# Kernel optimization log

Measured on AMD Instinct MI355X. Metric: run time of the kernel, lower is better.

Reference implementation:

```python
import jax, jax.numpy as jnp
import numpy as np

B, S, D = 16, 38, 1792          # batch, seq_len, d_model = 768 + 2*512
H, DK = 4, 448                   # heads, head dim (D // H)
NP = 128                         # prototype rows before repeat
TOPK = 3                         # hard-coded in VqaPrototypeModel
INF = 768                        # qamodel.qa_outputs.in_features


def setup_inputs() -> dict:
    key = jax.random.key(0)
    ks = jax.random.split(key, 16)
    sc = lambda d: 1.0 / np.sqrt(d)
    inp = {
        "combined_features": jax.random.normal(ks[0], (B, S, D), jnp.float32),
        "prototype_vectors": jax.random.normal(ks[1], (1, NP, D), jnp.float32),
        "attention_mask": jnp.ones((B, S), jnp.int32),
        # MultiThreadMemory: 4 Linear(d_model, d_model) -> q, k, v, out
        "Wq": jax.random.normal(ks[2], (D, D), jnp.float32) * sc(D),
        "bq": jnp.zeros((D,), jnp.float32),
        "Wk": jax.random.normal(ks[3], (D, D), jnp.float32) * sc(D),
        "bk": jnp.zeros((D,), jnp.float32),
        "Wv": jax.random.normal(ks[4], (D, D), jnp.float32) * sc(D),
        "bv": jnp.zeros((D,), jnp.float32),
        "Wo": jax.random.normal(ks[5], (D, D), jnp.float32) * sc(D),
        "bo": jnp.zeros((D,), jnp.float32),
        # fc: Linear(2*d_model, in_features)
        "Wfc": jax.random.normal(ks[6], (2 * D, INF), jnp.float32) * sc(2 * D),
        "bfc": jnp.zeros((INF,), jnp.float32),
        # stub of qamodel.qa_outputs: Linear(in_features, 2)
        "Wqa": jax.random.normal(ks[7], (INF, 2), jnp.float32) * sc(INF),
        "bqa": jnp.zeros((2,), jnp.float32),
    }
    return inp


def reference(combined_features, prototype_vectors, attention_mask,
              Wq, bq, Wk, bk, Wv, bv, Wo, bo, Wfc, bfc, Wqa, bqa):
    b, s, d = combined_features.shape
    # prototype_vectors.repeat(batch_size, seq_length, 1) -> [B, S*NP, D]
    pv = jnp.tile(prototype_vectors, (b, s, 1))
    m = pv.shape[1]

    q = combined_features @ Wq + bq                     # [B,S,D]
    k = pv @ Wk + bk                                    # [B,M,D]
    v = pv @ Wv + bv                                    # [B,M,D]

    q = q.reshape(b, s, H, DK).transpose(0, 2, 1, 3)    # [B,H,S,DK]
    k = k.reshape(b, m, H, DK).transpose(0, 2, 1, 3)    # [B,H,M,DK]
    v = v.reshape(b, m, H, DK).transpose(0, 2, 1, 3)    # [B,H,M,DK]

    # memory_querying_responding: score + topk + gather + softmax + weighted sum
    scores = jnp.einsum('bhsd,bhmd->bhsm', q, k) / np.sqrt(DK)  # [B,H,S,M]
    sel_scores, idx = jax.lax.top_k(scores, TOPK)               # [B,H,S,TOPK]
    # gather selected prototype values: v[b,h,idx[b,h,s,:],:]
    sel_value = jnp.take_along_axis(v[:, :, None, :, :], idx[..., None], axis=3)
    # sel_value: [B,H,S,TOPK,DK]
    p_attn = jax.nn.softmax(sel_scores.astype(jnp.float32), axis=-1)
    x = jnp.einsum('bhsk,bhskd->bhsd', p_attn, sel_value)       # [B,H,S,DK]
    x = x.transpose(0, 2, 1, 3).reshape(b, s, H * DK)           # [B,S,D]
    response = x @ Wo + bo

    final = jnp.concatenate([combined_features, response], axis=2)  # [B,S,2D]
    reduced = final @ Wfc + bfc                                     # [B,S,INF]
    # qamodel stub: qa_outputs head -> start/end logits stacked on last dim
    logits = reduced @ Wqa + bqa                                    # [B,S,2]
    return logits
```

## Files before the change

### kernel.cpp

```cpp
#include <hip/hip_runtime.h>

typedef __attribute__((ext_vector_type(8))) short short8v;
typedef __attribute__((ext_vector_type(4))) float f32x4;

#define APL 5120
#define BPL 5184
#define BBASE 15360

struct SP {
    const float *p0, *p1, *p2, *p3, *p4, *p5, *p6, *p7;
    float *q0, *q1, *q2;
};

__device__ __forceinline__ float wave_sum(float v) {
    #pragma unroll
    for (int off = 32; off; off >>= 1) v += __shfl_down(v, off);
    return v;
}

__device__ __forceinline__ void colvec2_unit(
    const float* __restrict__ A, int lda, const float* __restrict__ W,
    float* __restrict__ out, int K, int m, int lane)
{
    const float4* a = (const float4*)(A + (long)m * lda);
    float a0 = 0.f, a1 = 0.f;
    for (int i = 0; i < K / 256; ++i) {
        const int d4 = lane + 64 * i;
        float4 xv = a[d4];
        const float4* w = (const float4*)(W + (long)d4 * 8);
        float4 w0 = w[0], w1 = w[1];
        a0 += xv.x*w0.x + xv.y*w0.z + xv.z*w1.x + xv.w*w1.z;
        a1 += xv.x*w0.y + xv.y*w0.w + xv.z*w1.y + xv.w*w1.w;
    }
    a0 = wave_sum(a0); a1 = wave_sum(a1);
    if (lane == 0) { out[m * 2 + 0] = a0; out[m * 2 + 1] = a1; }
}

__device__ __forceinline__ void sbias_unit(
    const float* __restrict__ bq, const float* __restrict__ Kp,
    float* __restrict__ sb, int unit, int lane)
{
    const int h = unit >> 7, p = unit & 127;
    const float* kr = Kp + (long)p * 1792 + h * 448;
    const float* bh = bq + h * 448;
    float s = 0.f;
    #pragma unroll
    for (int i = 0; i < 7; ++i) s = fmaf(bh[lane + 64 * i], kr[lane + 64 * i], s);
    s = wave_sum(s);
    if (lane == 0) sb[unit] = s;
}

__device__ __forceinline__ void wvwoq_unit(
    const float* __restrict__ Wv, const float* __restrict__ WoQ,
    float* __restrict__ out, int d, int h, int lane)
{
    const float* wr = Wv + (long)d * 1792 + h * 448;
    const float* wq = WoQ + h * 448 * 2;
    float s0 = 0.f, s1 = 0.f;
    #pragma unroll
    for (int i = 0; i < 7; ++i) {
        const int j = lane + 64 * i;
        const float v = wr[j];
        s0 = fmaf(v, wq[j * 2 + 0], s0);
        s1 = fmaf(v, wq[j * 2 + 1], s1);
    }
    s0 = wave_sum(s0); s1 = wave_sum(s1);
    if (lane == 0) {
        out[((long)h * 1792 + d) * 2 + 0] = s0;
        out[((long)h * 1792 + d) * 2 + 1] = s1;
    }
}

__device__ __forceinline__ void bias_unit(
    const float* __restrict__ bv, const float* __restrict__ WoQ,
    const float* __restrict__ bfc, const float* __restrict__ Wqa,
    const float* __restrict__ bo, const float* __restrict__ WfbQ,
    const float* __restrict__ bqa,
    float* __restrict__ cv, float* __restrict__ const2, int unit, int lane)
{
    float s0 = 0.f, s1 = 0.f;
    if (unit < 4) {
        const int h = unit;
        #pragma unroll
        for (int i = 0; i < 7; ++i) {
            const int j = h * 448 + lane + 64 * i;
            const float v = bv[j];
            s0 = fmaf(v, WoQ[j * 2 + 0], s0);
            s1 = fmaf(v, WoQ[j * 2 + 1], s1);
        }
    } else {
        for (int k = lane; k < 1792; k += 64) {
            if (k < 768) {
                s0 = fmaf(bfc[k], Wqa[k * 2 + 0], s0);
                s1 = fmaf(bfc[k], Wqa[k * 2 + 1], s1);
            }
            s0 = fmaf(bo[k], WfbQ[k * 2 + 0], s0);
            s1 = fmaf(bo[k], WfbQ[k * 2 + 1], s1);
        }
    }
    s0 = wave_sum(s0); s1 = wave_sum(s1);
    if (lane == 0) {
        if (unit < 4) { cv[unit * 2 + 0] = s0; cv[unit * 2 + 1] = s1; }
        else          { const2[0] = s0 + bqa[0]; const2[1] = s1 + bqa[1]; }
    }
}

__device__ __forceinline__ void split3(float f, unsigned& h, unsigned& m, unsigned& l) {
    unsigned u = __float_as_uint(f);
    h = u >> 16;
    float r1 = f - __uint_as_float(u & 0xFFFF0000u);
    unsigned u1 = __float_as_uint(r1);
    m = u1 >> 16;
    float r2 = r1 - __uint_as_float(u1 & 0xFFFF0000u);
    l = __float_as_uint(r2) >> 16;
}

__device__ __forceinline__ int BROWF(int n) { return n * 40 + (n >> 4) * 8; }

template<bool TRANSB, int SIDE>
__global__ __launch_bounds__(256) void mgemm(
    const float* __restrict__ A, int lda,
    const float* __restrict__ B, int ldb,
    float* __restrict__ C,
    int M, int N, int K,
    int nsplit, int nbb, int mainZ,
    long sAb, long sBb, SP sp)
{
    const int tid = threadIdx.x;
    if ((int)blockIdx.z >= mainZ) {
        const int bid = ((int)blockIdx.z - mainZ) * (gridDim.x * gridDim.y)
                      + blockIdx.y * gridDim.x + blockIdx.x;
        const int lane = tid & 63;
        const int u = bid * 4 + (tid >> 6);
        if constexpr (SIDE == 1) {
            if (u < 3584) colvec2_unit(sp.p0, 768, sp.p1, sp.q0, 768, u, lane);
        } else if constexpr (SIDE == 2) {
            if (u < 1792)       colvec2_unit(sp.p0, 1792, sp.p1, sp.q0, 1792, u, lane);
            else if (u < 2304)  sbias_unit(sp.p2, sp.p3, sp.q1, u - 1792, lane);
        } else if constexpr (SIDE == 3) {
            if (u < 7168)       wvwoq_unit(sp.p0, sp.p1, sp.q0, u % 1792, u / 1792, lane);
            else if (u < 7173)  bias_unit(sp.p2, sp.p1, sp.p3, sp.p4, sp.p5, sp.p6, sp.p7,
                                          sp.q1, sp.q2, u - 7168, lane);
        }
        return;
    }

    __shared__ unsigned short sh[30912];

    const int kb = blockIdx.z % nsplit;
    const int bb = blockIdx.z / nsplit;
    A += sAb * bb;
    B += sBb * bb;
    const int Kc = K / nsplit;
    const int kbeg = kb * Kc;
    const int nsteps = Kc / 32;

    const int lane = tid & 63, wave = tid >> 6;
    const int g = lane >> 4, c = lane & 15;
    const int wm = (wave >> 1) * 64, wn = (wave & 1) * 64;
    const int rowBase = blockIdx.y * 128;
    const int colBase = blockIdx.x * 128;

    const int s_arow = tid >> 1, s_ak = (tid & 1) * 16;
    const int s_bk = tid >> 3,  s_bn = (tid & 7) * 16;
    const int s_tn = tid >> 1,  s_tk = (tid & 1) * 16;

    const bool aok = (rowBase + s_arow) < M;
    const float* Arow = A + (long)(rowBase + s_arow) * lda;

    float4 ra[4], rb[4];
    auto loadRaw = [&](int ks) {
        const int k0 = kbeg + ks * 32;
        #pragma unroll
        for (int i = 0; i < 4; ++i)
            ra[i] = aok ? *(const float4*)&Arow[k0 + s_ak + i * 4]
                        : make_float4(0.f, 0.f, 0.f, 0.f);
        if (!TRANSB) {
            const float* bp = B + (long)(k0 + s_bk) * ldb + colBase + s_bn;
            #pragma unroll
            for (int i = 0; i < 4; ++i) rb[i] = *(const float4*)&bp[i * 4];
        } else {
            const float* bp = B + (long)(colBase + s_tn) * ldb + k0 + s_tk;
            #pragma unroll
            for (int i = 0; i < 4; ++i) rb[i] = *(const float4*)&bp[i * 4];
        }
    };

    auto stageWrite = [&]() {
        {
            const float* f = (const float*)ra;
            unsigned ph[8], pm[8], pl[8];
            #pragma unroll
            for (int j = 0; j < 8; ++j) {
                unsigned h0, m0, l0, h1, m1, l1;
                split3(f[2*j], h0, m0, l0);
                split3(f[2*j+1], h1, m1, l1);
                ph[j] = h0 | (h1 << 16);
                pm[j] = m0 | (m1 << 16);
                pl[j] = l0 | (l1 << 16);
            }
            const int base = s_arow * 40 + s_ak;
            unsigned short* ap = sh;
            *(uint4*)&ap[0*APL + base]     = make_uint4(ph[0],ph[1],ph[2],ph[3]);
            *(uint4*)&ap[0*APL + base + 8] = make_uint4(ph[4],ph[5],ph[6],ph[7]);
            *(uint4*)&ap[1*APL + base]     = make_uint4(pm[0],pm[1],pm[2],pm[3]);
            *(uint4*)&ap[1*APL + base + 8] = make_uint4(pm[4],pm[5],pm[6],pm[7]);
            *(uint4*)&ap[2*APL + base]     = make_uint4(pl[0],pl[1],pl[2],pl[3]);
            *(uint4*)&ap[2*APL + base + 8] = make_uint4(pl[4],pl[5],pl[6],pl[7]);
        }
        unsigned short* bp = sh + BBASE;
        if (!TRANSB) {
            const float* f = (const float*)rb;
            #pragma unroll
            for (int j = 0; j < 16; ++j) {
                unsigned h, m, l;
                split3(f[j], h, m, l);
                const int ad = BROWF(s_bn + j) + s_bk;
                bp[0*BPL + ad] = (unsigned short)h;
                bp[1*BPL + ad] = (unsigned short)m;
                bp[2*BPL + ad] = (unsigned short)l;
            }
        } else {
            const float* f = (const float*)rb;
            unsigned ph[8], pm[8], pl[8];
            #pragma unroll
            for (int j = 0; j < 8; ++j) {
                unsigned h0, m0, l0, h1, m1, l1;
                split3(f[2*j], h0, m0, l0);
                split3(f[2*j+1], h1, m1, l1);
                ph[j] = h0 | (h1 << 16);
                pm[j] = m0 | (m1 << 16);
                pl[j] = l0 | (l1 << 16);
            }
            const int base = BROWF(s_tn) + s_tk;
            *(uint4*)&bp[0*BPL + base]     = make_uint4(ph[0],ph[1],ph[2],ph[3]);
            *(uint4*)&bp[0*BPL + base + 8] = make_uint4(ph[4],ph[5],ph[6],ph[7]);
            *(uint4*)&bp[1*BPL + base]     = make_uint4(pm[0],pm[1],pm[2],pm[3]);
            *(uint4*)&bp[1*BPL + base + 8] = make_uint4(pm[4],pm[5],pm[6],pm[7]);
            *(uint4*)&bp[2*BPL + base]     = make_uint4(pl[0],pl[1],pl[2],pl[3]);
            *(uint4*)&bp[2*BPL + base + 8] = make_uint4(pl[4],pl[5],pl[6],pl[7]);
        }
    };

    f32x4 acc[4][4];
    #pragma unroll
    for (int i = 0; i < 4; ++i)
        #pragma unroll
        for (int j = 0; j < 4; ++j)
            acc[i][j] = (f32x4){0.f, 0.f, 0.f, 0.f};

    loadRaw(0);
    for (int s = 0; s < nsteps; ++s) {
        __syncthreads();
        stageWrite();
        if (s + 1 < nsteps) loadRaw(s + 1);
        __syncthreads();

        const unsigned short* ap = sh;
        const unsigned short* bp = sh + BBASE;
        short8v bfr[3][4];
        #pragma unroll
        for (int ni = 0; ni < 4; ++ni) {
            const int hwb = (wn + 16*ni + c) * 40 + ((wn + 16*ni) >> 4) * 8 + 8 * g;
            bfr[0][ni] = *(const short8v*)&bp[0*BPL + hwb];
            bfr[1][ni] = *(const short8v*)&bp[1*BPL + hwb];
            bfr[2][ni] = *(const short8v*)&bp[2*BPL + hwb];
        }
        #pragma unroll
        for (int mi = 0; mi < 4; ++mi) {
            const int hwa = (wm + 16*mi + c) * 40 + 8 * g;
            short8v ah = *(const short8v*)&ap[0*APL + hwa];
            short8v am = *(const short8v*)&ap[1*APL + hwa];
            short8v al = *(const short8v*)&ap[2*APL + hwa];
            #pragma unroll
            for (int ni = 0; ni < 4; ++ni) {
                f32x4 t = acc[mi][ni];
                t = __builtin_amdgcn_mfma_f32_16x16x32_bf16(ah, bfr[0][ni], t, 0, 0, 0);
                t = __builtin_amdgcn_mfma_f32_16x16x32_bf16(ah, bfr[1][ni], t, 0, 0, 0);
                t = __builtin_amdgcn_mfma_f32_16x16x32_bf16(am, bfr[0][ni], t, 0, 0, 0);
                t = __builtin_amdgcn_mfma_f32_16x16x32_bf16(ah, bfr[2][ni], t, 0, 0, 0);
                t = __builtin_amdgcn_mfma_f32_16x16x32_bf16(am, bfr[1][ni], t, 0, 0, 0);
                t = __builtin_amdgcn_mfma_f32_16x16x32_bf16(al, bfr[0][ni], t, 0, 0, 0);
                acc[mi][ni] = t;
            }
        }
    }

    float* Cw = C + ((long)kb * nbb + bb) * (long)M * N;
    #pragma unroll
    for (int mi = 0; mi < 4; ++mi)
        #pragma unroll
        for (int ni = 0; ni < 4; ++ni) {
            const int col = colBase + wn + 16*ni + c;
            #pragma unroll
            for (int r = 0; r < 4; ++r) {
                const int row = rowBase + wm + 16*mi + 4*g + r;
                if (row < M) Cw[(long)row * N + col] = acc[mi][ni][r];
            }
        }
}

__global__ __launch_bounds__(256) void reduce_add(
    const float* __restrict__ part, float* __restrict__ out,
    const float* __restrict__ bias, int N, long sz, int nsplit)
{
    long i = (long)blockIdx.x * 256 + threadIdx.x;
    const long stride = (long)gridDim.x * 256;
    for (; i < sz; i += stride) {
        float s = 0.f;
        for (int z = 0; z < nsplit; ++z) s += part[z * sz + i];
        if (bias) s += bias[i % N];
        out[i] = s;
    }
}

__global__ __launch_bounds__(256) void argmax_final_k(
    const float* __restrict__ Sp,
    const float* __restrict__ sbias,
    const float* __restrict__ X, const float* __restrict__ Wbig,
    const float* __restrict__ WvWoQ,
    const float* __restrict__ proto,
    const float* __restrict__ cv, const float* __restrict__ const2,
    float* __restrict__ out)
{
    const int lane = threadIdx.x & 63;
    const int row = blockIdx.x * 4 + (threadIdx.x >> 6);
    if (row >= 608) return;

    int sel[4];
    #pragma unroll
    for (int h = 0; h < 4; ++h) {
        float s0 = sbias[h * 128 + lane];
        float s1 = sbias[h * 128 + lane + 64];
        #pragma unroll
        for (int z = 0; z < 8; ++z) {
            const long base = ((long)(z * 4 + h) * 608 + row) * 128;
            s0 += Sp[base + lane];
            s1 += Sp[base + lane + 64];
        }
        float best = s0; int bi = lane;
        if (s1 > best) { best = s1; bi = lane + 64; }
        #pragma unroll
        for (int off = 32; off; off >>= 1) {
            float ov = __shfl_down(best, off);
            int   oi = __shfl_down(bi, off);
            if (ov > best || (ov == best && oi < bi)) { best = ov; bi = oi; }
        }
        sel[h] = __shfl(bi, 0);
    }

    float a0 = 0.f, a1 = 0.f;
    auto dot2 = [&](const float* a, const float* w) {
        const float4* av = (const float4*)a;
        #pragma unroll
        for (int i = 0; i < 7; ++i) {
            const int d4 = lane + 64 * i;
            float4 xv = av[d4];
            const float4* wp = (const float4*)(w + (long)d4 * 8);
            float4 w0 = wp[0], w1 = wp[1];
            a0 += xv.x*w0.x + xv.y*w0.z + xv.z*w1.x + xv.w*w1.z;
            a1 += xv.x*w0.y + xv.y*w0.w + xv.z*w1.y + xv.w*w1.w;
        }
    };
    dot2(X + (long)row * 1792, Wbig);
    #pragma unroll
    for (int h = 0; h < 4; ++h)
        dot2(proto + (long)sel[h] * 1792, WvWoQ + (long)h * 3584);

    a0 = wave_sum(a0); a1 = wave_sum(a1);
    if (lane == 0) {
        out[row * 2 + 0] = a0 + const2[0] + cv[0] + cv[2] + cv[4] + cv[6];
        out[row * 2 + 1] = a1 + const2[1] + cv[1] + cv[3] + cv[5] + cv[7];
    }
}

extern "C" void kernel_launch(void* const* d_in, const int* in_sizes, int n_in,
                              void* d_out, int out_size, void* d_ws, size_t ws_size,
                              hipStream_t stream)
{
    const float* X     = (const float*)d_in[0];
    const float* proto = (const float*)d_in[1];
    const float* Wq  = (const float*)d_in[3];
    const float* bq  = (const float*)d_in[4];
    const float* Wk  = (const float*)d_in[5];
    const float* bk  = (const float*)d_in[6];
    const float* Wv  = (const float*)d_in[7];
    const float* bv  = (const float*)d_in[8];
    const float* Wo  = (const float*)d_in[9];
    const float* bo  = (const float*)d_in[10];
    const float* Wfc = (const float*)d_in[11];
    const float* bfc = (const float*)d_in[12];
    const float* Wqa = (const float*)d_in[13];
    const float* bqa = (const float*)d_in[14];
    float* out = (float*)d_out;

    float* ws = (float*)d_ws;
    float* P      = ws;
    float* Kp     = P + 3211264;
    float* W2b    = Kp + 229376;
    float* sbias  = W2b + 917504;
    float* WbigB  = sbias + 512;
    float* WoQ    = WbigB + 7168;
    float* WvWoQ  = WoQ + 3584;
    float* cv     = WvWoQ + 14336;
    float* const2 = cv + 8;
    float* WfbQ   = WbigB + 3584;

    dim3 blk(256);

    {
        SP sp{}; sp.p0 = Wfc; sp.p1 = Wqa; sp.q0 = WbigB;
        mgemm<false, 1><<<dim3(14, 1, 14 + 64), blk, 0, stream>>>(
            proto, 1792, Wk, 1792, P, 128, 1792, 1792, 14, 1, 14, 0, 0, sp);
    }
    reduce_add<<<dim3(896), blk, 0, stream>>>(P, Kp, bk, 1792, 229376L, 14);

    {
        SP sp{}; sp.p0 = Wo; sp.p1 = WfbQ; sp.q0 = WoQ; sp.p2 = bq; sp.p3 = Kp; sp.q1 = sbias;
        mgemm<true, 2><<<dim3(1, 14, 8 + 42), blk, 0, stream>>>(
            Wq, 1792, Kp, 1792, P, 1792, 128, 448, 2, 4, 8, 448, 448, sp);
    }
    reduce_add<<<dim3(1792), blk, 0, stream>>>(P, W2b, nullptr, 1, 917504L, 2);

    {
        SP sp{}; sp.p0 = Wv; sp.p1 = WoQ; sp.q0 = WvWoQ;
        sp.p2 = bv; sp.p3 = bfc; sp.p4 = Wqa; sp.p5 = bo; sp.p6 = WfbQ; sp.p7 = bqa;
        sp.q1 = cv; sp.q2 = const2;
        mgemm<false, 3><<<dim3(1, 5, 32 + 359), blk, 0, stream>>>(
            X, 1792, W2b, 128, P, 608, 128, 1792, 8, 4, 32, 0, 229376L, sp);
    }
    argmax_final_k<<<dim3(152), blk, 0, stream>>>(
        P, sbias, X, WbigB, WvWoQ, proto, cv, const2, out);
}
```

Baseline: 81.05 us.

## Fuse all stages into one cooperative persistent kernel with grid syncs

Replaces the six separate kernel launches (three GEMMs with side work plus two reductions and the final argmax) with a single cooperative persistent kernel that runs six phases separated by grid-wide barriers. Work is redistributed: the split-K is raised (14 splits in the last GEMM), and reductions plus side vector products are interleaved inside phases via grid-stride loops. The aim is to remove launch overhead and inter-kernel gaps. It risks grid.sync costs, a grid capped at 448 blocks limiting parallelism, and extra partial-sum traffic. A fallback launches the phases as separate kernels.

```diff
diff --git a/kernel.cpp b/kernel.cpp
--- a/kernel.cpp
+++ b/kernel.cpp
@@ -1,4 +1,7 @@
 #include <hip/hip_runtime.h>
+#include <hip/hip_cooperative_groups.h>
+
+namespace cg = cooperative_groups;
 
 typedef __attribute__((ext_vector_type(8))) short short8v;
 typedef __attribute__((ext_vector_type(4))) float f32x4;
@@ -6,10 +9,11 @@
 #define APL 5120
 #define BPL 5184
 #define BBASE 15360
-
-struct SP {
-    const float *p0, *p1, *p2, *p3, *p4, *p5, *p6, *p7;
-    float *q0, *q1, *q2;
+#define MAXGRID 448
+
+struct MA {
+    const float *X, *proto, *Wq, *bq, *Wk, *bk, *Wv, *bv, *Wo, *bo, *Wfc, *bfc, *Wqa, *bqa;
+    float *P, *Kp, *W2b, *sbias, *WbigB, *WoQ, *WvWoQ, *cv, *const2, *out;
 };
 
 __device__ __forceinline__ float wave_sum(float v) {
@@ -117,49 +121,17 @@
 
 __device__ __forceinline__ int BROWF(int n) { return n * 40 + (n >> 4) * 8; }
 
-template<bool TRANSB, int SIDE>
-__global__ __launch_bounds__(256) void mgemm(
+template<bool TRANSB>
+__device__ void gemm_tile(unsigned short* sh,
     const float* __restrict__ A, int lda,
     const float* __restrict__ B, int ldb,
-    float* __restrict__ C,
-    int M, int N, int K,
-    int nsplit, int nbb, int mainZ,
-    long sAb, long sBb, SP sp)
+    float* __restrict__ Cslab, int M, int N,
+    int rowBase, int colBase, int kbeg, int nsteps)
 {
     const int tid = threadIdx.x;
-    if ((int)blockIdx.z >= mainZ) {
-        const int bid = ((int)blockIdx.z - mainZ) * (gridDim.x * gridDim.y)
-                      + blockIdx.y * gridDim.x + blockIdx.x;
-        const int lane = tid & 63;
-        const int u = bid * 4 + (tid >> 6);
-        if constexpr (SIDE == 1) {
-            if (u < 3584) colvec2_unit(sp.p0, 768, sp.p1, sp.q0, 768, u, lane);
-        } else if constexpr (SIDE == 2) {
-            if (u < 1792)       colvec2_unit(sp.p0, 1792, sp.p1, sp.q0, 1792, u, lane);
-            else if (u < 2304)  sbias_unit(sp.p2, sp.p3, sp.q1, u - 1792, lane);
-        } else if constexpr (SIDE == 3) {
-            if (u < 7168)       wvwoq_unit(sp.p0, sp.p1, sp.q0, u % 1792, u / 1792, lane);
-            else if (u < 7173)  bias_unit(sp.p2, sp.p1, sp.p3, sp.p4, sp.p5, sp.p6, sp.p7,
-                                          sp.q1, sp.q2, u - 7168, lane);
-        }
-        return;
-    }
-
-    __shared__ unsigned short sh[30912];
-
-    const int kb = blockIdx.z % nsplit;
-    const int bb = blockIdx.z / nsplit;
-    A += sAb * bb;
-    B += sBb * bb;
-    const int Kc = K / nsplit;
-    const int kbeg = kb * Kc;
-    const int nsteps = Kc / 32;
-
     const int lane = tid & 63, wave = tid >> 6;
     const int g = lane >> 4, c = lane & 15;
     const int wm = (wave >> 1) * 64, wn = (wave & 1) * 64;
-    const int rowBase = blockIdx.y * 128;
-    const int colBase = blockIdx.x * 128;
 
     const int s_arow = tid >> 1, s_ak = (tid & 1) * 16;
     const int s_bk = tid >> 3,  s_bn = (tid & 7) * 16;
@@ -286,7 +258,6 @@
         }
     }
 
-    float* Cw = C + ((long)kb * nbb + bb) * (long)M * N;
     #pragma unroll
     for (int mi = 0; mi < 4; ++mi)
         #pragma unroll
@@ -295,140 +266,224 @@
             #pragma unroll
             for (int r = 0; r < 4; ++r) {
                 const int row = rowBase + wm + 16*mi + 4*g + r;
-                if (row < M) Cw[(long)row * N + col] = acc[mi][ni][r];
-            }
-        }
-}
-
-__global__ __launch_bounds__(256) void reduce_add(
-    const float* __restrict__ part, float* __restrict__ out,
-    const float* __restrict__ bias, int N, long sz, int nsplit)
-{
-    long i = (long)blockIdx.x * 256 + threadIdx.x;
-    const long stride = (long)gridDim.x * 256;
-    for (; i < sz; i += stride) {
-        float s = 0.f;
-        for (int z = 0; z < nsplit; ++z) s += part[z * sz + i];
-        if (bias) s += bias[i % N];
-        out[i] = s;
-    }
-}
-
-__global__ __launch_bounds__(256) void argmax_final_k(
-    const float* __restrict__ Sp,
-    const float* __restrict__ sbias,
-    const float* __restrict__ X, const float* __restrict__ Wbig,
-    const float* __restrict__ WvWoQ,
-    const float* __restrict__ proto,
-    const float* __restrict__ cv, const float* __restrict__ const2,
-    float* __restrict__ out)
-{
-    const int lane = threadIdx.x & 63;
-    const int row = blockIdx.x * 4 + (threadIdx.x >> 6);
-    if (row >= 608) return;
-
-    int sel[4];
-    #pragma unroll
-    for (int h = 0; h < 4; ++h) {
-        float s0 = sbias[h * 128 + lane];
-        float s1 = sbias[h * 128 + lane + 64];
-        #pragma unroll
-        for (int z = 0; z < 8; ++z) {
-            const long base = ((long)(z * 4 + h) * 608 + row) * 128;
-            s0 += Sp[base + lane];
-            s1 += Sp[base + lane + 64];
-        }
-        float best = s0; int bi = lane;
-        if (s1 > best) { best = s1; bi = lane + 64; }
-        #pragma unroll
-        for (int off = 32; off; off >>= 1) {
-            float ov = __shfl_down(best, off);
-            int   oi = __shfl_down(bi, off);
-            if (ov > best || (ov == best && oi < bi)) { best = ov; bi = oi; }
-        }
-        sel[h] = __shfl(bi, 0);
-    }
-
-    float a0 = 0.f, a1 = 0.f;
-    auto dot2 = [&](const float* a, const float* w) {
-        const float4* av = (const float4*)a;
-        #pragma unroll
-        for (int i = 0; i < 7; ++i) {
-            const int d4 = lane + 64 * i;
-            float4 xv = av[d4];
-            const float4* wp = (const float4*)(w + (long)d4 * 8);
-            float4 w0 = wp[0], w1 = wp[1];
-            a0 += xv.x*w0.x + xv.y*w0.z + xv.z*w1.x + xv.w*w1.z;
-            a1 += xv.x*w0.y + xv.y*w0.w + xv.z*w1.y + xv.w*w1.w;
-        }
-    };
-    dot2(X + (long)row * 1792, Wbig);
-    #pragma unroll
-    for (int h = 0; h < 4; ++h)
-        dot2(proto + (long)sel[h] * 1792, WvWoQ + (long)h * 3584);
-
-    a0 = wave_sum(a0); a1 = wave_sum(a1);
-    if (lane == 0) {
-        out[row * 2 + 0] = a0 + const2[0] + cv[0] + cv[2] + cv[4] + cv[6];
-        out[row * 2 + 1] = a1 + const2[1] + cv[1] + cv[3] + cv[5] + cv[7];
-    }
-}
+                if (row < M) Cslab[(long)row * N + col] = acc[mi][ni][r];
+            }
+        }
+}
+
+
+__device__ void phaseA(const MA& a, unsigned short* sh) {
+    const int lane = threadIdx.x & 63, wave = threadIdx.x >> 6;
+    for (int w = blockIdx.x; w < 196 + 448; w += gridDim.x) {
+        if (w < 196) {
+            const int kb = w % 14, tx = w / 14;
+            gemm_tile<false>(sh, a.proto, 1792, a.Wk, 1792,
+                             a.P + (long)kb * 229376, 128, 1792,
+                             0, tx * 128, kb * 128, 4);
+        } else {
+            const int u = (w - 196) * 4 + wave;
+            if (u < 1792) colvec2_unit(a.Wfc + 1792L * 768, 768, a.Wqa,
+                                       a.WbigB + 3584, 768, u, lane);
+        }
+    }
+}
+
+__device__ void phaseB(const MA& a) {
+    const int lane = threadIdx.x & 63, wave = threadIdx.x >> 6;
+    for (int w = blockIdx.x; w < 224 + 448; w += gridDim.x) {
+        if (w < 224) {
+            const long i0 = (long)w * 1024 + threadIdx.x * 4;
+            float4 s = make_float4(0.f, 0.f, 0.f, 0.f);
+            for (int z = 0; z < 14; ++z) {
+                float4 v = *(const float4*)&a.P[z * 229376L + i0];
+                s.x += v.x; s.y += v.y; s.z += v.z; s.w += v.w;
+            }
+            const int col = (int)(i0 % 1792);
+            float4 b4 = *(const float4*)&a.bk[col];
+            s.x += b4.x; s.y += b4.y; s.z += b4.z; s.w += b4.w;
+            *(float4*)&a.Kp[i0] = s;
+        } else {
+            const int u = (w - 224) * 4 + wave;
+            if (u < 1792) colvec2_unit(a.Wo, 1792, a.WbigB + 3584, a.WoQ, 1792, u, lane);
+        }
+    }
+}
+
+__device__ void phaseC(const MA& a, unsigned short* sh) {
+    const int lane = threadIdx.x & 63, wave = threadIdx.x >> 6;
+    for (int w = blockIdx.x; w < 1136; w += gridDim.x) {
+        if (w < 112) {
+            const int kb = w & 1, r = w >> 1, bb = r & 3, ty = r >> 2;
+            gemm_tile<true>(sh, a.Wq + 448 * bb, 1792, a.Kp + 448 * bb, 1792,
+                            a.P + (long)(kb * 4 + bb) * 229376, 1792, 128,
+                            ty * 128, 0, kb * 224, 7);
+        } else if (w < 240) {
+            const int u = (w - 112) * 4 + wave;
+            if (u < 512) sbias_unit(a.bq, a.Kp, a.sbias, u, lane);
+        } else {
+            const int u = (w - 240) * 4 + wave;
+            if (u < 3584) wvwoq_unit(a.Wv, a.WoQ, a.WvWoQ, u % 1792, u / 1792, lane);
+        }
+    }
+}
+
+__device__ void phaseD(const MA& a) {
+    const int lane = threadIdx.x & 63, wave = threadIdx.x >> 6;
+    for (int w = blockIdx.x; w < 1794; w += gridDim.x) {
+        if (w < 896) {
+            const long i0 = (long)w * 1024 + threadIdx.x * 4;
+            float4 v0 = *(const float4*)&a.P[i0];
+            float4 v1 = *(const float4*)&a.P[917504L + i0];
+            *(float4*)&a.W2b[i0] = make_float4(v0.x + v1.x, v0.y + v1.y,
+                                               v0.z + v1.z, v0.w + v1.w);
+        } else if (w < 1792) {
+            const int u = (w - 896) * 4 + wave;
+            if (u < 3584) {
+                const int unit = 3584 + u;
+                wvwoq_unit(a.Wv, a.WoQ, a.WvWoQ, unit % 1792, unit / 1792, lane);
+            }
+        } else {
+            const int u = (w - 1792) * 4 + wave;
+            if (u < 5) bias_unit(a.bv, a.WoQ, a.bfc, a.Wqa, a.bo, a.WbigB + 3584,
+                                 a.bqa, a.cv, a.const2, u, lane);
+        }
+    }
+}
+
+__device__ void phaseE(const MA& a, unsigned short* sh) {
+    const int lane = threadIdx.x & 63, wave = threadIdx.x >> 6;
+    for (int w = blockIdx.x; w < 280 + 448; w += gridDim.x) {
+        if (w < 280) {
+            const int kb = w % 14, r = w / 14, bb = r & 3, ty = r >> 2;
+            gemm_tile<false>(sh, a.X, 1792, a.W2b + 229376L * bb, 128,
+                             a.P + (long)(kb * 4 + bb) * 77824, 608, 128,
+                             ty * 128, 0, kb * 128, 4);
+        } else {
+            const int u = (w - 280) * 4 + wave;
+            if (u < 1792) colvec2_unit(a.Wfc, 768, a.Wqa, a.WbigB, 768, u, lane);
+        }
+    }
+}
+
+__device__ void phaseF(const MA& a) {
+    const int lane = threadIdx.x & 63, wave = threadIdx.x >> 6;
+    for (int w = blockIdx.x; w < 152; w += gridDim.x) {
+        const int row = w * 4 + wave;
+
+        int sel[4];
+        #pragma unroll
+        for (int h = 0; h < 4; ++h) {
+            float s0 = a.sbias[h * 128 + lane];
+            float s1 = a.sbias[h * 128 + lane + 64];
+            #pragma unroll 2
+            for (int z = 0; z < 14; ++z) {
+                const long base = ((long)(z * 4 + h) * 608 + row) * 128;
+                s0 += a.P[base + lane];
+                s1 += a.P[base + lane + 64];
+            }
+            float best = s0; int bi = lane;
+            if (s1 > best) { best = s1; bi = lane + 64; }
+            #pragma unroll
+            for (int off = 32; off; off >>= 1) {
+                float ov = __shfl_down(best, off);
+                int   oi = __shfl_down(bi, off);
+                if (ov > best || (ov == best && oi < bi)) { best = ov; bi = oi; }
+            }
+            sel[h] = __shfl(bi, 0);
+        }
+
+        float a0 = 0.f, a1 = 0.f;
+        auto dot2 = [&](const float* av_, const float* w_) {
+            const float4* av = (const float4*)av_;
+            #pragma unroll
+            for (int i = 0; i < 7; ++i) {
+                const int d4 = lane + 64 * i;
+                float4 xv = av[d4];
+                const float4* wp = (const float4*)(w_ + (long)d4 * 8);
+                float4 w0 = wp[0], w1 = wp[1];
+                a0 += xv.x*w0.x + xv.y*w0.z + xv.z*w1.x + xv.w*w1.z;
+                a1 += xv.x*w0.y + xv.y*w0.w + xv.z*w1.y + xv.w*w1.w;
+            }
+        };
+        dot2(a.X + (long)row * 1792, a.WbigB);
+        #pragma unroll
+        for (int h = 0; h < 4; ++h)
+            dot2(a.proto + (long)sel[h] * 1792, a.WvWoQ + (long)h * 3584);
+
+        a0 = wave_sum(a0); a1 = wave_sum(a1);
+        if (lane == 0) {
+            a.out[row * 2 + 0] = a0 + a.const2[0] + a.cv[0] + a.cv[2] + a.cv[4] + a.cv[6];
+            a.out[row * 2 + 1] = a1 + a.const2[1] + a.cv[1] + a.cv[3] + a.cv[5] + a.cv[7];
+        }
+    }
+}
+
+__global__ __launch_bounds__(256, 2) void mega(MA a) {
+    __shared__ unsigned short sh[30912];
+    cg::grid_group grid = cg::this_grid();
+    phaseA(a, sh);  grid.sync();
+    phaseB(a);      grid.sync();
+    phaseC(a, sh);  grid.sync();
+    phaseD(a);      grid.sync();
+    phaseE(a, sh);  grid.sync();
+    phaseF(a);
+}
+
+__global__ __launch_bounds__(256) void phA_k(MA a) { __shared__ unsigned short sh[30912]; phaseA(a, sh); }
+__global__ __launch_bounds__(256) void phB_k(MA a) { phaseB(a); }
+__global__ __launch_bounds__(256) void phC_k(MA a) { __shared__ unsigned short sh[30912]; phaseC(a, sh); }
+__global__ __launch_bounds__(256) void phD_k(MA a) { phaseD(a); }
+__global__ __launch_bounds__(256) void phE_k(MA a) { __shared__ unsigned short sh[30912]; phaseE(a, sh); }
+__global__ __launch_bounds__(256) void phF_k(MA a) { phaseF(a); }
 
 extern "C" void kernel_launch(void* const* d_in, const int* in_sizes, int n_in,
                               void* d_out, int out_size, void* d_ws, size_t ws_size,
                               hipStream_t stream)
 {
-    const float* X     = (const float*)d_in[0];
-    const float* proto = (const float*)d_in[1];
-    const float* Wq  = (const float*)d_in[3];
-    const float* bq  = (const float*)d_in[4];
-    const float* Wk  = (const float*)d_in[5];
-    const float* bk  = (const float*)d_in[6];
-    const float* Wv  = (const float*)d_in[7];
-    const float* bv  = (const float*)d_in[8];
-    const float* Wo  = (const float*)d_in[9];
-    const float* bo  = (const float*)d_in[10];
-    const float* Wfc = (const float*)d_in[11];
-    const float* bfc = (const float*)d_in[12];
-    const float* Wqa = (const float*)d_in[13];
-    const float* bqa = (const float*)d_in[14];
-    float* out = (float*)d_out;
+    MA a;
+    a.X     = (const float*)d_in[0];
+    a.proto = (const float*)d_in[1];
+    a.Wq  = (const float*)d_in[3];
+    a.bq  = (const float*)d_in[4];
+    a.Wk  = (const float*)d_in[5];
+    a.bk  = (const float*)d_in[6];
+    a.Wv  = (const float*)d_in[7];
+    a.bv  = (const float*)d_in[8];
+    a.Wo  = (const float*)d_in[9];
+    a.bo  = (const float*)d_in[10];
+    a.Wfc = (const float*)d_in[11];
+    a.bfc = (const float*)d_in[12];
+    a.Wqa = (const float*)d_in[13];
+    a.bqa = (const float*)d_in[14];
+    a.out = (float*)d_out;
 
     float* ws = (float*)d_ws;
-    float* P      = ws;
-    float* Kp     = P + 3211264;
-    float* W2b    = Kp + 229376;
-    float* sbias  = W2b + 917504;
-    float* WbigB  = sbias + 512;
-    float* WoQ    = WbigB + 7168;
-    float* WvWoQ  = WoQ + 3584;
-    float* cv     = WvWoQ + 14336;
-    float* const2 = cv + 8;
-    float* WfbQ   = WbigB + 3584;
-
-    dim3 blk(256);
-
-    {
-        SP sp{}; sp.p0 = Wfc; sp.p1 = Wqa; sp.q0 = WbigB;
-        mgemm<false, 1><<<dim3(14, 1, 14 + 64), blk, 0, stream>>>(
-            proto, 1792, Wk, 1792, P, 128, 1792, 1792, 14, 1, 14, 0, 0, sp);
-    }
-    reduce_add<<<dim3(896), blk, 0, stream>>>(P, Kp, bk, 1792, 229376L, 14);
-
-    {
-        SP sp{}; sp.p0 = Wo; sp.p1 = WfbQ; sp.q0 = WoQ; sp.p2 = bq; sp.p3 = Kp; sp.q1 = sbias;
-        mgemm<true, 2><<<dim3(1, 14, 8 + 42), blk, 0, stream>>>(
-            Wq, 1792, Kp, 1792, P, 1792, 128, 448, 2, 4, 8, 448, 448, sp);
-    }
-    reduce_add<<<dim3(1792), blk, 0, stream>>>(P, W2b, nullptr, 1, 917504L, 2);
-
-    {
-        SP sp{}; sp.p0 = Wv; sp.p1 = WoQ; sp.q0 = WvWoQ;
-        sp.p2 = bv; sp.p3 = bfc; sp.p4 = Wqa; sp.p5 = bo; sp.p6 = WfbQ; sp.p7 = bqa;
-        sp.q1 = cv; sp.q2 = const2;
-        mgemm<false, 3><<<dim3(1, 5, 32 + 359), blk, 0, stream>>>(
-            X, 1792, W2b, 128, P, 608, 128, 1792, 8, 4, 32, 0, 229376L, sp);
-    }
-    argmax_final_k<<<dim3(152), blk, 0, stream>>>(
-        P, sbias, X, WbigB, WvWoQ, proto, cv, const2, out);
-}
+    a.P      = ws;
+    a.Kp     = a.P + 4358144;
+    a.W2b    = a.Kp + 229376;
+    a.sbias  = a.W2b + 917504;
+    a.WbigB  = a.sbias + 512;
+    a.WoQ    = a.WbigB + 7168;
+    a.WvWoQ  = a.WoQ + 3584;
+    a.cv     = a.WvWoQ + 14336;
+    a.const2 = a.cv + 8;
+
+    int maxB = 0;
+    hipError_t qe = hipOccupancyMaxActiveBlocksPerMultiprocessor(&maxB, mega, 256, 0);
+    bool coopOK = (qe == hipSuccess && maxB >= 1);
+    if (coopOK) {
+        int grid = maxB * 256;
+        if (grid > MAXGRID) grid = MAXGRID;
+        void* params[] = { (void*)&a };
+        hipError_t e = hipLaunchCooperativeKernel((const void*)mega, dim3(grid), dim3(256),
+                                                  params, 0, stream);
+        if (e == hipSuccess) return;
+        (void)hipGetLastError();
+    }
+    phA_k<<<dim3(MAXGRID), 256, 0, stream>>>(a);
+    phB_k<<<dim3(MAXGRID), 256, 0, stream>>>(a);
+    phC_k<<<dim3(MAXGRID), 256, 0, stream>>>(a);
+    phD_k<<<dim3(MAXGRID), 256, 0, stream>>>(a);
+    phE_k<<<dim3(MAXGRID), 256, 0, stream>>>(a);
+    phF_k<<<dim3(MAXGRID), 256, 0, stream>>>(a);
+}
```

New measurement: 131.1 us. 1.62x slower.
